# Performance work log

Measured on AMD Instinct MI355X. Metric: run time of the kernel, lower is better.

The kernel has to match this reference:

```python
import jax, jax.numpy as jnp
import numpy as np

NUM_HEADS = 16

def setup_inputs() -> dict:
    key = jax.random.key(0)
    ks = jax.random.split(key, 6)
    C = 512
    nW, B, N = 64, 4, 144
    x = jax.random.normal(ks[0], (B * nW, N, C), dtype=jnp.float32)
    mask = jax.random.randint(ks[1], (nW, N, N), 0, 2, dtype=jnp.int32)
    Wqkv = jax.random.normal(ks[2], (C, 3 * C), dtype=jnp.float32) * (1.0 / np.sqrt(C))
    bqkv = jnp.zeros((3 * C,), dtype=jnp.float32)
    Wproj = jax.random.normal(ks[3], (C, C), dtype=jnp.float32) * (1.0 / np.sqrt(C))
    bproj = jnp.zeros((C,), dtype=jnp.float32)
    return {"x": x, "mask": mask, "Wqkv": Wqkv, "bqkv": bqkv, "Wproj": Wproj, "bproj": bproj}

def reference(x, mask, Wqkv, bqkv, Wproj, bproj):
    Bn, N, C = x.shape
    H = NUM_HEADS
    D = C // H
    nW = mask.shape[0]
    B = Bn // nW
    scale = 1.0 / jnp.sqrt(jnp.asarray(D, dtype=x.dtype))

    qkv = x @ Wqkv + bqkv                        # (Bn, N, 3C)
    qkv = qkv.reshape(Bn, N, 3, H, D)            # packed order (qkv, H, D)
    qkv = jnp.transpose(qkv, (2, 0, 3, 1, 4))    # (3, Bn, H, N, D)
    q, k, v = qkv[0], qkv[1], qkv[2]

    # split window-batch dim: (B nW) -> B, nW
    q = q.reshape(B, nW, H, N, D)
    k = k.reshape(B, nW, H, N, D)
    v = v.reshape(B, nW, H, N, D)

    attn = jnp.einsum('bwhnd,bwhmd->bwhnm', q, k) * scale
    bias = jnp.where(mask == 0, -jnp.inf, 0.0).astype(x.dtype)  # (nW, N, N)
    attn = attn + bias.reshape(1, nW, 1, N, N)
    attn = jax.nn.softmax(attn, axis=-1)

    out = jnp.einsum('bwhnm,bwhmd->bwhnd', attn, v)   # (B, nW, H, N, D)
    out = jnp.transpose(out, (0, 1, 3, 2, 4)).reshape(Bn, N, C)
    return out @ Wproj + bproj
```

## Files before the change

### kernel.cpp

```cpp
#include <hip/hip_runtime.h>

typedef unsigned short u16;
typedef unsigned int u32;
typedef unsigned long long u64;
typedef __attribute__((ext_vector_type(4))) float f32x4;
typedef __attribute__((ext_vector_type(8))) short bf16x8;
typedef __attribute__((ext_vector_type(4))) u32 u32x4;

__device__ __forceinline__ u16 f2bf(float f) {
  union { float f; u32 u; } v; v.f = f;
  u32 r = v.u + 0x7fffu + ((v.u >> 16) & 1u);
  return (u16)(r >> 16);
}

__device__ __forceinline__ u16 f2bf_rne(float f) {
  u32 w;
  asm("v_cvt_pk_bf16_f32 %0, %1, %2" : "=v"(w) : "v"(f), "v"(f));
  return (u16)w;
}

__device__ __forceinline__ void gload_lds16(const u16* g, u16* l) {
  __builtin_amdgcn_global_load_lds((__attribute__((address_space(1))) const void*)g,
                                   (__attribute__((address_space(3))) void*)l,
                                   16, 0, 0);
}

__global__ void __launch_bounds__(256) k_transpose_w(const float* __restrict__ W,
                                                     u16* __restrict__ Wt, int K, int Nc) {
  __shared__ u16 t[64][72];
  const int tid = threadIdx.x;
  const int kb = blockIdx.x * 64, nb = blockIdx.y * 64;
  const int c4 = (tid & 15) * 4;
  const int r0 = tid >> 4;
#pragma unroll
  for (int rr = 0; rr < 4; ++rr) {
    int r = rr * 16 + r0;
    float4 v = *(const float4*)(W + (size_t)(kb + r) * Nc + nb + c4);
    t[r][c4 + 0] = f2bf(v.x);
    t[r][c4 + 1] = f2bf(v.y);
    t[r][c4 + 2] = f2bf(v.z);
    t[r][c4 + 3] = f2bf(v.w);
  }
  __syncthreads();
  const int c8 = (tid & 7) * 8;
  const int rn = tid >> 3;
#pragma unroll
  for (int rr = 0; rr < 2; ++rr) {
    int n = rr * 32 + rn;
    u16 tmp[8];
#pragma unroll
    for (int j = 0; j < 8; ++j) tmp[j] = t[c8 + j][n];
    *(u32x4*)(Wt + (size_t)(nb + n) * K + kb + c8) = *(const u32x4*)tmp;
  }
}

__global__ void __launch_bounds__(256) k_mask_bits(const int* __restrict__ mask,
                                                   u32* __restrict__ mtab) {
  const int row = blockIdx.x * 4 + (threadIdx.x >> 6);
  const int lane = threadIdx.x & 63;
  const int* base = mask + (size_t)row * 144;
  u64 b01 = __ballot(base[lane] != 0);
  u64 b23 = __ballot(base[64 + lane] != 0);
  int v4 = (lane < 16) ? base[128 + lane] : 0;
  u64 b4 = __ballot(v4 != 0);
  if (lane == 0) {
    u32* o = mtab + (size_t)row * 8;
    o[0] = (u32)b01; o[1] = (u32)(b01 >> 32);
    o[2] = (u32)b23; o[3] = (u32)(b23 >> 32);
    o[4] = (u32)b4;  o[5] = 0; o[6] = 0; o[7] = 0;
  }
}

template <bool OUT_BF16, bool A_FP32>
__global__ void __launch_bounds__(512, 2) k_gemm(const void* __restrict__ Ap,
                                                 const u16* __restrict__ Bt,
                                                 const float* __restrict__ bias,
                                                 void* __restrict__ D,
                                                 int Nc, int K, int NB) {
  __shared__ u16 As[256 * 68];
  __shared__ u16 Bs[2][128 * 64];
  const int tid = threadIdx.x;
  const int wave = tid >> 6, lane = tid & 63;
  const int wr = wave >> 1, wc = wave & 1;
  const int l15 = lane & 15, g = lane >> 4;
  const int sx = l15 & 7;
  const f32x4 fzero = {0.f, 0.f, 0.f, 0.f};

  const int cpx = gridDim.x >> 3;
  const int swz = (blockIdx.x & 7) * cpx + (blockIdx.x >> 3);
  const int bm = swz / NB, bn = swz % NB;

  const u16* Bb = Bt + (size_t)bn * 128 * K;

  int rr[4], cc[4];
#pragma unroll
  for (int i = 0; i < 4; ++i) {
    int e = i * 512 + tid;
    rr[i] = e >> 3;
    cc[i] = e & 7;
  }

  f32x4 acc[4][4];
#pragma unroll
  for (int m = 0; m < 4; ++m)
#pragma unroll
    for (int n = 0; n < 4; ++n) acc[m][n] = fzero;

  f32x4 areg[8];
  u32x4 aregb[4];

  auto A_LOAD = [&](int ks) {
    if constexpr (A_FP32) {
      const float* Af = (const float*)Ap;
#pragma unroll
      for (int i = 0; i < 4; ++i) {
        const float* p = Af + (size_t)(bm * 256 + rr[i]) * K + ks + cc[i] * 8;
        areg[2 * i] = *(const f32x4*)(p);
        areg[2 * i + 1] = *(const f32x4*)(p + 4);
      }
    } else {
      const u16* Ab = (const u16*)Ap + (size_t)bm * 256 * K;
#pragma unroll
      for (int i = 0; i < 4; ++i)
        aregb[i] = *(const u32x4*)(Ab + (size_t)rr[i] * K + ks + cc[i] * 8);
    }
  };

  auto A_WRITE = [&]() {
#pragma unroll
    for (int i = 0; i < 4; ++i) {
      u32x4 wv;
      if constexpr (A_FP32) {
        u32 w0, w1, w2, w3;
        asm("v_cvt_pk_bf16_f32 %0, %1, %2" : "=v"(w0) : "v"(areg[2 * i][0]), "v"(areg[2 * i][1]));
        asm("v_cvt_pk_bf16_f32 %0, %1, %2" : "=v"(w1) : "v"(areg[2 * i][2]), "v"(areg[2 * i][3]));
        asm("v_cvt_pk_bf16_f32 %0, %1, %2" : "=v"(w2) : "v"(areg[2 * i + 1][0]), "v"(areg[2 * i + 1][1]));
        asm("v_cvt_pk_bf16_f32 %0, %1, %2" : "=v"(w3) : "v"(areg[2 * i + 1][2]), "v"(areg[2 * i + 1][3]));
        wv[0] = w0; wv[1] = w1; wv[2] = w2; wv[3] = w3;
      } else {
        wv = aregb[i];
      }
      *(u32x4*)(&As[rr[i] * 68 + cc[i] * 8]) = wv;
    }
  };

  auto B_STAGE = [&](int buf, int ks) {
#pragma unroll
    for (int i = 0; i < 2; ++i) {
      int e = i * 512 + tid;
      int r = e >> 3, c = e & 7;
      int cs = c ^ (r & 7);
      gload_lds16(Bb + (size_t)r * K + ks + (cs << 3), &Bs[buf][e * 8]);
    }
  };

  auto COMPUTE = [&](int buf) {
#pragma unroll
    for (int kk = 0; kk < 2; ++kk) {
      bf16x8 a[4], b[4];
#pragma unroll
      for (int m = 0; m < 4; ++m)
        a[m] = *(const bf16x8*)(&As[(wr * 64 + m * 16 + l15) * 68 + (kk * 4 + g) * 8]);
#pragma unroll
      for (int n = 0; n < 4; ++n)
        b[n] = *(const bf16x8*)(&Bs[buf][(wc * 64 + n * 16 + l15) * 64 + (((kk * 4 + g) ^ sx) << 3)]);
#pragma unroll
      for (int m = 0; m < 4; ++m)
#pragma unroll
        for (int n = 0; n < 4; ++n)
          acc[m][n] = __builtin_amdgcn_mfma_f32_16x16x32_bf16(a[m], b[n], acc[m][n], 0, 0, 0);
    }
  };

  const int nt = K >> 6;
  A_LOAD(0);
  B_STAGE(0, 0);
  int cur = 0;
  for (int t = 0; t < nt; ++t) {
    asm volatile("s_waitcnt vmcnt(0)" ::: "memory");
    __builtin_amdgcn_sched_barrier(0);
    if (t + 1 < nt) B_STAGE(cur ^ 1, (t + 1) << 6);
    A_WRITE();
    if (t + 1 < nt) A_LOAD((t + 1) << 6);
    asm volatile("s_waitcnt lgkmcnt(0)" ::: "memory");
    __builtin_amdgcn_sched_barrier(0);
    __builtin_amdgcn_s_barrier();
    __builtin_amdgcn_sched_barrier(0);
    COMPUTE(cur);
    __builtin_amdgcn_sched_barrier(0);
    if (t + 1 < nt) __builtin_amdgcn_s_barrier();
    cur ^= 1;
  }

  const int row0 = bm * 256 + wr * 64;
  const int col0 = bn * 128 + wc * 64;
#pragma unroll
  for (int m = 0; m < 4; ++m) {
#pragma unroll
    for (int n = 0; n < 4; ++n) {
      int col = col0 + n * 16 + l15;
      float bv = bias[col];
#pragma unroll
      for (int j = 0; j < 4; ++j) {
        int row = row0 + m * 16 + g * 4 + j;
        float v = acc[m][n][j] + bv;
        if constexpr (OUT_BF16)
          ((u16*)D)[(size_t)row * Nc + col] = f2bf_rne(v);
        else
          ((float*)D)[(size_t)row * Nc + col] = v;
      }
    }
  }
}

__global__ void __launch_bounds__(192) k_attn(const u16* __restrict__ qkv,
                                              const u32* __restrict__ mtab,
                                              u16* __restrict__ obuf) {
  __shared__ u16 k_s[144 * 40];
  __shared__ u16 vT_s[32 * 168];
  __shared__ u16 P_s[3][16 * 168];

  const int bh = blockIdx.x;
  const int bn = bh >> 4, h = bh & 15;
  const int wid = bn & 63;
  const int tid = threadIdx.x;
  const int wave = tid >> 6, lane = tid & 63;
  const int l15 = lane & 15, g = lane >> 4;
  const f32x4 fzero = {0.f, 0.f, 0.f, 0.f};

  const u16* base = qkv + (size_t)bn * 144 * 1536 + h * 32;
  u16* Pw = &P_s[wave][0];

  bf16x8 qb[3];
  u32 mw[3][5];
#pragma unroll
  for (int it = 0; it < 3; ++it) {
    const int mt = wave + it * 3;
    qb[it] = *(const bf16x8*)(base + (size_t)(mt * 16 + l15) * 1536 + g * 8);
    const u32* mp = mtab + ((size_t)(wid * 144 + mt * 16 + l15) << 3);
#pragma unroll
    for (int wd = 0; wd < 5; ++wd) mw[it][wd] = mp[wd];
  }

  *(u32*)(Pw + l15 * 168 + 144 + g * 4) = 0;
  *(u32*)(Pw + l15 * 168 + 144 + g * 4 + 2) = 0;

  for (int e = tid; e < 576; e += 192) {
    int n = e >> 2, c = e & 3;
    const u16* rowp = base + (size_t)n * 1536 + c * 8;
    u32x4 kv = *(const u32x4*)(rowp + 512);
    u32x4 vv = *(const u32x4*)(rowp + 1024);
    *(u32x4*)(k_s + n * 40 + c * 8) = kv;
#pragma unroll
    for (int t = 0; t < 4; ++t) {
      u32 w = vv[t];
      vT_s[(c * 8 + 2 * t) * 168 + n] = (u16)(w & 0xffffu);
      vT_s[(c * 8 + 2 * t + 1) * 168 + n] = (u16)(w >> 16);
    }
  }
  for (int e = tid; e < 512; e += 192) {
    int d = e >> 4, c = e & 15;
    vT_s[d * 168 + 144 + c] = 0;
  }
  __syncthreads();

  const float scale = 0.17677669529663687f;

  f32x4 accs[9];
  float rinv;

#define QKT(IT)                                                                  \
  {                                                                              \
    _Pragma("unroll") for (int nt = 0; nt < 9; ++nt) {                           \
      bf16x8 kf = *(const bf16x8*)(k_s + (nt * 16 + l15) * 40 + g * 8);          \
      accs[nt] = __builtin_amdgcn_mfma_f32_16x16x32_bf16(kf, qb[IT], fzero, 0, 0, 0); \
    }                                                                            \
  }
#define SM(IT)                                                                   \
  {                                                                              \
    float rsum = 0.f;                                                            \
    _Pragma("unroll") for (int nt = 0; nt < 9; ++nt) {                           \
      const int wd = nt >> 1;                                                    \
      const int shb = (nt & 1) * 16;                                             \
      _Pragma("unroll") for (int j = 0; j < 4; ++j) {                            \
        float e = __expf(accs[nt][j] * scale);                                   \
        u32 bit = (mw[IT][wd] >> (shb + g * 4 + j)) & 1u;                        \
        e = bit ? e : 0.f;                                                       \
        accs[nt][j] = e;                                                         \
        rsum += e;                                                               \
      }                                                                          \
    }                                                                            \
    rsum += __shfl_xor(rsum, 16, 64);                                            \
    rsum += __shfl_xor(rsum, 32, 64);                                            \
    rinv = 1.f / rsum;                                                           \
  }

  QKT(0);
  SM(0);

#pragma unroll
  for (int it = 0; it < 3; ++it) {
    const int mt = wave + it * 3;

#pragma unroll
    for (int nt = 0; nt < 9; ++nt) {
      u32 w0, w1;
      float p0 = accs[nt][0] * rinv, p1 = accs[nt][1] * rinv;
      float p2 = accs[nt][2] * rinv, p3 = accs[nt][3] * rinv;
      asm("v_cvt_pk_bf16_f32 %0, %1, %2" : "=v"(w0) : "v"(p0), "v"(p1));
      asm("v_cvt_pk_bf16_f32 %0, %1, %2" : "=v"(w1) : "v"(p2), "v"(p3));
      *(u32*)(Pw + l15 * 168 + nt * 16 + g * 4) = w0;
      *(u32*)(Pw + l15 * 168 + nt * 16 + g * 4 + 2) = w1;
    }

    if (it == 0) QKT(1);
    if (it == 1) QKT(2);

    asm volatile("s_waitcnt lgkmcnt(0)" ::: "memory");
    __builtin_amdgcn_sched_barrier(0);

    f32x4 acco[2];
    acco[0] = fzero;
    acco[1] = fzero;
    __builtin_amdgcn_s_setprio(1);
#pragma unroll
    for (int kk = 0; kk < 5; ++kk) {
      bf16x8 pa = *(const bf16x8*)(Pw + l15 * 168 + kk * 32 + g * 8);
#pragma unroll
      for (int nt2 = 0; nt2 < 2; ++nt2) {
        bf16x8 b = *(const bf16x8*)(vT_s + (nt2 * 16 + l15) * 168 + kk * 32 + g * 8);
        acco[nt2] = __builtin_amdgcn_mfma_f32_16x16x32_bf16(pa, b, acco[nt2], 0, 0, 0);
      }
    }
    __builtin_amdgcn_s_setprio(0);

    if (it == 0) SM(1);
    if (it == 1) SM(2);

#pragma unroll
    for (int nt2 = 0; nt2 < 2; ++nt2)
#pragma unroll
      for (int j = 0; j < 4; ++j) {
        int r = mt * 16 + g * 4 + j;
        int d = nt2 * 16 + l15;
        obuf[((size_t)bn * 144 + r) * 512 + h * 32 + d] = f2bf_rne(acco[nt2][j]);
      }
  }
#undef QKT
#undef SM
}

extern "C" void kernel_launch(void* const* d_in, const int* in_sizes, int n_in,
                              void* d_out, int out_size, void* d_ws, size_t ws_size,
                              hipStream_t stream) {
  const float* x = (const float*)d_in[0];
  const int* mask = (const int*)d_in[1];
  const float* Wqkv = (const float*)d_in[2];
  const float* bqkv = (const float*)d_in[3];
  const float* Wproj = (const float*)d_in[4];
  const float* bproj = (const float*)d_in[5];
  float* out = (float*)d_out;

  char* ws = (char*)d_ws;
  u32* mtab    = (u32*)(ws + 0);
  u16* wqkv_t  = (u16*)(ws + 294912);
  u16* qkv     = (u16*)(ws + 1867776);
  u16* obuf    = (u16*)(ws + 115113984);
  u16* wproj_t = (u16*)(ws + 152862720);

  k_transpose_w<<<dim3(8, 24), 256, 0, stream>>>(Wqkv, wqkv_t, 512, 1536);
  k_transpose_w<<<dim3(8, 8), 256, 0, stream>>>(Wproj, wproj_t, 512, 512);
  k_mask_bits<<<2304, 256, 0, stream>>>(mask, mtab);
  k_gemm<true, true><<<1728, 512, 0, stream>>>(x, wqkv_t, bqkv, qkv, 1536, 512, 12);
  k_attn<<<4096, 192, 0, stream>>>(qkv, mtab, obuf);
  k_gemm<false, false><<<576, 512, 0, stream>>>(obuf, wproj_t, bproj, out, 512, 512, 4);
}
```

Before: 229.4 us.

## Shrink GEMM tiles to 128x128 with double-buffered A and deeper prefetch

Halves the GEMM block tile from 256x128 to 128x128 with 256 threads, doubling the grid. A is now double-buffered in LDS, and the loop is restructured so the next tile's B stage and A write overlap the current compute, with finer vmcnt waits instead of full drains. The attention softmax also switches from __expf with a natural scale to exp2f with a log2e-prefolded scale. This reduces A reuse per block and adds LDS and register pressure in exchange for more parallelism and better load/compute overlap.

```diff
diff --git a/kernel.cpp b/kernel.cpp
--- a/kernel.cpp
+++ b/kernel.cpp
@@ -72,12 +72,12 @@
 }
 
 template <bool OUT_BF16, bool A_FP32>
-__global__ void __launch_bounds__(512, 2) k_gemm(const void* __restrict__ Ap,
+__global__ void __launch_bounds__(256, 2) k_gemm(const void* __restrict__ Ap,
                                                  const u16* __restrict__ Bt,
                                                  const float* __restrict__ bias,
                                                  void* __restrict__ D,
                                                  int Nc, int K, int NB) {
-  __shared__ u16 As[256 * 68];
+  __shared__ u16 As[2][128 * 68];
   __shared__ u16 Bs[2][128 * 64];
   const int tid = threadIdx.x;
   const int wave = tid >> 6, lane = tid & 63;
@@ -95,7 +95,7 @@
   int rr[4], cc[4];
 #pragma unroll
   for (int i = 0; i < 4; ++i) {
-    int e = i * 512 + tid;
+    int e = i * 256 + tid;
     rr[i] = e >> 3;
     cc[i] = e & 7;
   }
@@ -114,19 +114,19 @@
       const float* Af = (const float*)Ap;
 #pragma unroll
       for (int i = 0; i < 4; ++i) {
-        const float* p = Af + (size_t)(bm * 256 + rr[i]) * K + ks + cc[i] * 8;
+        const float* p = Af + (size_t)(bm * 128 + rr[i]) * K + ks + cc[i] * 8;
         areg[2 * i] = *(const f32x4*)(p);
         areg[2 * i + 1] = *(const f32x4*)(p + 4);
       }
     } else {
-      const u16* Ab = (const u16*)Ap + (size_t)bm * 256 * K;
+      const u16* Ab = (const u16*)Ap + (size_t)bm * 128 * K;
 #pragma unroll
       for (int i = 0; i < 4; ++i)
         aregb[i] = *(const u32x4*)(Ab + (size_t)rr[i] * K + ks + cc[i] * 8);
     }
   };
 
-  auto A_WRITE = [&]() {
+  auto A_WRITE = [&](int buf) {
 #pragma unroll
     for (int i = 0; i < 4; ++i) {
       u32x4 wv;
@@ -140,17 +140,15 @@
       } else {
         wv = aregb[i];
       }
-      *(u32x4*)(&As[rr[i] * 68 + cc[i] * 8]) = wv;
+      *(u32x4*)(&As[buf][rr[i] * 68 + cc[i] * 8]) = wv;
     }
   };
 
   auto B_STAGE = [&](int buf, int ks) {
 #pragma unroll
-    for (int i = 0; i < 2; ++i) {
-      int e = i * 512 + tid;
-      int r = e >> 3, c = e & 7;
-      int cs = c ^ (r & 7);
-      gload_lds16(Bb + (size_t)r * K + ks + (cs << 3), &Bs[buf][e * 8]);
+    for (int i = 0; i < 4; ++i) {
+      int cs = cc[i] ^ (rr[i] & 7);
+      gload_lds16(Bb + (size_t)rr[i] * K + ks + (cs << 3), &Bs[buf][(i * 256 + tid) * 8]);
     }
   };
 
@@ -160,7 +158,7 @@
       bf16x8 a[4], b[4];
 #pragma unroll
       for (int m = 0; m < 4; ++m)
-        a[m] = *(const bf16x8*)(&As[(wr * 64 + m * 16 + l15) * 68 + (kk * 4 + g) * 8]);
+        a[m] = *(const bf16x8*)(&As[buf][(wr * 64 + m * 16 + l15) * 68 + (kk * 4 + g) * 8]);
 #pragma unroll
       for (int n = 0; n < 4; ++n)
         b[n] = *(const bf16x8*)(&Bs[buf][(wc * 64 + n * 16 + l15) * 64 + (((kk * 4 + g) ^ sx) << 3)]);
@@ -175,24 +173,43 @@
   const int nt = K >> 6;
   A_LOAD(0);
   B_STAGE(0, 0);
+  asm volatile("s_waitcnt vmcnt(4)" ::: "memory");
+  __builtin_amdgcn_sched_barrier(0);
+  A_WRITE(0);
+  if (nt > 1) A_LOAD(64);
+  if constexpr (A_FP32)
+    asm volatile("s_waitcnt vmcnt(8) lgkmcnt(0)" ::: "memory");
+  else
+    asm volatile("s_waitcnt vmcnt(4) lgkmcnt(0)" ::: "memory");
+  __builtin_amdgcn_sched_barrier(0);
+  __builtin_amdgcn_s_barrier();
+  __builtin_amdgcn_sched_barrier(0);
+
   int cur = 0;
   for (int t = 0; t < nt; ++t) {
-    asm volatile("s_waitcnt vmcnt(0)" ::: "memory");
-    __builtin_amdgcn_sched_barrier(0);
     if (t + 1 < nt) B_STAGE(cur ^ 1, (t + 1) << 6);
-    A_WRITE();
-    if (t + 1 < nt) A_LOAD((t + 1) << 6);
-    asm volatile("s_waitcnt lgkmcnt(0)" ::: "memory");
-    __builtin_amdgcn_sched_barrier(0);
-    __builtin_amdgcn_s_barrier();
-    __builtin_amdgcn_sched_barrier(0);
     COMPUTE(cur);
-    __builtin_amdgcn_sched_barrier(0);
-    if (t + 1 < nt) __builtin_amdgcn_s_barrier();
+    if (t + 1 < nt) {
+      asm volatile("s_waitcnt vmcnt(4)" ::: "memory");
+      __builtin_amdgcn_sched_barrier(0);
+      A_WRITE(cur ^ 1);
+      if (t + 2 < nt) {
+        A_LOAD((t + 2) << 6);
+        if constexpr (A_FP32)
+          asm volatile("s_waitcnt vmcnt(8) lgkmcnt(0)" ::: "memory");
+        else
+          asm volatile("s_waitcnt vmcnt(4) lgkmcnt(0)" ::: "memory");
+      } else {
+        asm volatile("s_waitcnt vmcnt(0) lgkmcnt(0)" ::: "memory");
+      }
+      __builtin_amdgcn_sched_barrier(0);
+      __builtin_amdgcn_s_barrier();
+      __builtin_amdgcn_sched_barrier(0);
+    }
     cur ^= 1;
   }
 
-  const int row0 = bm * 256 + wr * 64;
+  const int row0 = bm * 128 + wr * 64;
   const int col0 = bn * 128 + wc * 64;
 #pragma unroll
   for (int m = 0; m < 4; ++m) {
@@ -264,7 +281,7 @@
   }
   __syncthreads();
 
-  const float scale = 0.17677669529663687f;
+  const float SC2 = 0.25503487f;
 
   f32x4 accs[9];
   float rinv;
@@ -283,7 +300,7 @@
       const int wd = nt >> 1;                                                    \
       const int shb = (nt & 1) * 16;                                             \
       _Pragma("unroll") for (int j = 0; j < 4; ++j) {                            \
-        float e = __expf(accs[nt][j] * scale);                                   \
+        float e = exp2f(accs[nt][j] * SC2);                                      \
         u32 bit = (mw[IT][wd] >> (shb + g * 4 + j)) & 1u;                        \
         e = bit ? e : 0.f;                                                       \
         accs[nt][j] = e;                                                         \
@@ -371,7 +388,7 @@
   k_transpose_w<<<dim3(8, 24), 256, 0, stream>>>(Wqkv, wqkv_t, 512, 1536);
   k_transpose_w<<<dim3(8, 8), 256, 0, stream>>>(Wproj, wproj_t, 512, 512);
   k_mask_bits<<<2304, 256, 0, stream>>>(mask, mtab);
-  k_gemm<true, true><<<1728, 512, 0, stream>>>(x, wqkv_t, bqkv, qkv, 1536, 512, 12);
+  k_gemm<true, true><<<3456, 256, 0, stream>>>(x, wqkv_t, bqkv, qkv, 1536, 512, 12);
   k_attn<<<4096, 192, 0, stream>>>(qkv, mtab, obuf);
-  k_gemm<false, false><<<576, 512, 0, stream>>>(obuf, wproj_t, bproj, out, 512, 512, 4);
-}
+  k_gemm<false, false><<<1152, 256, 0, stream>>>(obuf, wproj_t, bproj, out, 512, 512, 4);
+}
```

New measurement: 229.3 us. About the same (-0.0%).
